# Performance work log

Measured on AMD Instinct MI355X. Metric: run time of the kernel, lower is better.

Reference implementation:

```python
import jax, jax.numpy as jnp
import numpy as np

IN_CH = 4096
OUT_CH = 11008
W_BITS = 4


def unpack_weight(qweight, wbit):
    # qweight: [in_ch * wbit // 32, out_ch] int32 -> intweight: [in_ch, out_ch] int32
    rows, cols = qweight.shape
    n = rows * (32 // wbit)
    i = jnp.arange(n)
    idx = (i * wbit) // 32            # which packed word each row comes from
    off = (i * wbit) % 32             # bit offset within the word
    # wbit=4 divides 32, so every value lies inside one word (simple path only)
    shift = (32 - off - wbit).astype(jnp.int32)
    mask = jnp.int32((1 << wbit) - 1)
    return jnp.bitwise_and(jnp.right_shift(qweight[idx], shift[:, None]), mask)


def setup_inputs() -> dict:
    key = jax.random.key(0)
    k1, k2, k3, k4 = jax.random.split(key, 4)
    x = jax.random.normal(k1, (4, 2048, IN_CH), dtype=jnp.float32)
    pack_weight = jax.random.randint(k2, (IN_CH * W_BITS // 32, OUT_CH), 0, 2**31 - 1, dtype=jnp.int32)
    w_scale = jax.random.uniform(k3, (OUT_CH, 1), dtype=jnp.float32) * 0.01 + 1e-3
    w_zero_point = jax.random.uniform(k4, (OUT_CH, 1), dtype=jnp.float32) * 15.0
    return {"x": x, "pack_weight": pack_weight, "w_scale": w_scale, "w_zero_point": w_zero_point}


def reference(x, pack_weight, w_scale, w_zero_point):
    # unpack int4 -> [in, out], transpose to [out, in] like w.t() in torch
    intw = unpack_weight(pack_weight, W_BITS).T.astype(x.dtype)  # [out, in]
    # per-channel dequant: scale/zero are [out, 1]
    w = (intw - w_zero_point) * w_scale                          # [out, in]
    # F.linear(x, w): x @ w.T
    return jnp.einsum('bsi,oi->bso', x, w)
```

## Files before the change

kernel.cpp:

```cpp
#include <hip/hip_runtime.h>
#include <hip/hip_bf16.h>


#define K_DIM 4096
#define N_DIM 11008
#define M_DIM 8192
#define LDA 40

typedef __attribute__((ext_vector_type(8))) short short8;
typedef __attribute__((ext_vector_type(4))) float f32x4;
typedef __attribute__((ext_vector_type(4))) unsigned int u32x4;

__global__ __launch_bounds__(256, 3) void qgemm_fused(
    const float* __restrict__ X, const int* __restrict__ Q,
    const float* __restrict__ SC, const float* __restrict__ ZP,
    float* __restrict__ C)
{
    __shared__ short As[128 * LDA];
    __shared__ short Bs[128 * LDA];

    const int tid  = threadIdx.x;
    const int lane = tid & 63;
    const int wave = tid >> 6;

    const int m0 = blockIdx.y * 128;
    const int n0 = blockIdx.x * 128;

    const int arow = tid >> 2;
    const int ak8  = (tid & 3) * 8;
    const float* xbase = X + (size_t)(m0 + arow) * K_DIM + ak8;

    const int bcol  = tid & 127;
    const int brow0 = tid >> 7;
    const int* qbase = Q + (size_t)brow0 * N_DIM + n0 + bcol;
    const float sc  = SC[n0 + bcol];
    const float nzs = -ZP[n0 + bcol] * sc;

    f32x4 areg[4];
    int   breg[2];

    auto load_tile = [&](int kt) {
        const float* p0 = xbase + kt;
        areg[0] = *(const f32x4*)(p0);
        areg[1] = *(const f32x4*)(p0 + 4);
        const float* p1 = p0 + (size_t)64 * K_DIM;
        areg[2] = *(const f32x4*)(p1);
        areg[3] = *(const f32x4*)(p1 + 4);
        const int* q0 = qbase + (size_t)(kt >> 3) * N_DIM;
        breg[0] = q0[0];
        breg[1] = q0[2 * N_DIM];
    };

    auto cvt2 = [&](float a, float b) -> unsigned {
        __hip_bfloat162 h = __float22bfloat162_rn(make_float2(a, b));
        unsigned u;
        __builtin_memcpy(&u, &h, 4);
        return u;
    };

    auto store_tile = [&]() {
        #pragma unroll
        for (int p = 0; p < 2; ++p) {
            u32x4 v;
            v[0] = cvt2(areg[2*p+0][0], areg[2*p+0][1]);
            v[1] = cvt2(areg[2*p+0][2], areg[2*p+0][3]);
            v[2] = cvt2(areg[2*p+1][0], areg[2*p+1][1]);
            v[3] = cvt2(areg[2*p+1][2], areg[2*p+1][3]);
            *(u32x4*)&As[(arow + p * 64) * LDA + ak8] = v;
        }
        #pragma unroll
        for (int r = 0; r < 2; ++r) {
            const unsigned w = (unsigned)breg[r];
            float f[8];
            #pragma unroll
            for (int j = 0; j < 8; ++j)
                f[j] = fmaf((float)((w >> (28 - 4*j)) & 15u), sc, nzs);
            u32x4 v;
            v[0] = cvt2(f[0], f[1]);
            v[1] = cvt2(f[2], f[3]);
            v[2] = cvt2(f[4], f[5]);
            v[3] = cvt2(f[6], f[7]);
            *(u32x4*)&Bs[bcol * LDA + (brow0 + 2*r) * 8] = v;
        }
    };

    f32x4 acc[4][4] = {};

    const int wm = (wave >> 1) * 64;
    const int wn = (wave & 1) * 64;
    const int fr = lane & 15;
    const int fq = lane >> 4;

    const short* Abase = &As[(wm + fr) * LDA + fq * 8];
    const short* Bbase = &Bs[(wn + fr) * LDA + fq * 8];

    load_tile(0);
    store_tile();
    __syncthreads();

    for (int kt = 0;;) {
        const int knext = kt + 32;
        const bool last = (knext >= K_DIM);
        if (!last) load_tile(knext);

        short8 af[4], bf[4];
        #pragma unroll
        for (int i = 0; i < 4; ++i) {
            af[i] = *(const short8*)(Abase + i * 16 * LDA);
            bf[i] = *(const short8*)(Bbase + i * 16 * LDA);
        }
        #pragma unroll
        for (int mi = 0; mi < 4; ++mi)
            #pragma unroll
            for (int ni = 0; ni < 4; ++ni)
                acc[mi][ni] = __builtin_amdgcn_mfma_f32_16x16x32_bf16(
                    af[mi], bf[ni], acc[mi][ni], 0, 0, 0);

        if (last) break;
        __syncthreads();
        store_tile();
        __syncthreads();
        kt = knext;
    }

    #pragma unroll
    for (int mi = 0; mi < 4; ++mi) {
        #pragma unroll
        for (int ni = 0; ni < 4; ++ni) {
            const int row = m0 + wm + mi * 16 + fq * 4;
            const int col = n0 + wn + ni * 16 + fr;
            float* cp = C + (size_t)row * N_DIM + col;
            #pragma unroll
            for (int r = 0; r < 4; ++r)
                cp[(size_t)r * N_DIM] = acc[mi][ni][r];
        }
    }
}

extern "C" void kernel_launch(void* const* d_in, const int* in_sizes, int n_in,
                              void* d_out, int out_size, void* d_ws, size_t ws_size,
                              hipStream_t stream) {
    const float* X  = (const float*)d_in[0];
    const int*   Q  = (const int*)d_in[1];
    const float* SC = (const float*)d_in[2];
    const float* ZP = (const float*)d_in[3];
    float*       C  = (float*)d_out;
    (void)d_ws; (void)ws_size; (void)in_sizes; (void)n_in; (void)out_size;

    qgemm_fused<<<dim3(N_DIM / 128, M_DIM / 128), 256, 0, stream>>>(X, Q, SC, ZP, C);
}
```

Measured before the change: 1.336 ms.

## Pre-convert X and dequantize weights into workspace, then run async-LDS GEMM

Splits the fused kernel into three launches. The first converts X to bf16 and the second dequantizes the int4 weights into a transposed bf16 [N,K] buffer, both written to the workspace. The third is a GEMM that streams tiles directly from global memory into double-buffered, XOR-swizzled LDS with global_load_lds. This removes the per-tile conversion and dequant work that every block repeated, and lets loads overlap compute. In exchange it costs extra global traffic and two extra launches, and it needs enough workspace, falling back to the old fused kernel otherwise.

New measurement: 1.671 ms. 25.1% more time.

```diff
diff --git a/kernel.cpp b/kernel.cpp
--- a/kernel.cpp
+++ b/kernel.cpp
@@ -5,12 +5,143 @@
 #define K_DIM 4096
 #define N_DIM 11008
 #define M_DIM 8192
-#define LDA 40
-
+#define BK 32
+
+typedef unsigned short u16;
 typedef __attribute__((ext_vector_type(8))) short short8;
 typedef __attribute__((ext_vector_type(4))) float f32x4;
 typedef __attribute__((ext_vector_type(4))) unsigned int u32x4;
 
+__device__ __forceinline__ unsigned cvt2(float a, float b) {
+    __hip_bfloat162 h = __float22bfloat162_rn(make_float2(a, b));
+    unsigned u;
+    __builtin_memcpy(&u, &h, 4);
+    return u;
+}
+
+#define GLOAD_LDS16(g, l)                                                 \
+    __builtin_amdgcn_global_load_lds(                                     \
+        (const __attribute__((address_space(1))) unsigned int*)(g),       \
+        (__attribute__((address_space(3))) unsigned int*)(l), 16, 0, 0)
+
+__global__ __launch_bounds__(256) void xcvt(const float* __restrict__ X,
+                                            u16* __restrict__ Xb) {
+    const size_t i = ((size_t)blockIdx.x * 256 + threadIdx.x) * 8;
+    f32x4 a = *(const f32x4*)(X + i);
+    f32x4 b = *(const f32x4*)(X + i + 4);
+    u32x4 v;
+    v[0] = cvt2(a[0], a[1]);
+    v[1] = cvt2(a[2], a[3]);
+    v[2] = cvt2(b[0], b[1]);
+    v[3] = cvt2(b[2], b[3]);
+    *(u32x4*)(Xb + i) = v;
+}
+
+__global__ __launch_bounds__(256) void wdeq(const int* __restrict__ Q,
+                                            const float* __restrict__ SC,
+                                            const float* __restrict__ ZP,
+                                            u16* __restrict__ Wt) {
+    const int t  = threadIdx.x;
+    const int n  = blockIdx.x * 32 + (t >> 3);
+    const int kw = blockIdx.y * 8 + (t & 7);
+    const unsigned w = (unsigned)Q[(size_t)kw * N_DIM + n];
+    const float sc  = SC[n];
+    const float nzs = -ZP[n] * sc;
+    float f[8];
+#pragma unroll
+    for (int j = 0; j < 8; ++j)
+        f[j] = fmaf((float)((w >> (28 - 4 * j)) & 15u), sc, nzs);
+    u32x4 v;
+    v[0] = cvt2(f[0], f[1]);
+    v[1] = cvt2(f[2], f[3]);
+    v[2] = cvt2(f[4], f[5]);
+    v[3] = cvt2(f[6], f[7]);
+    *(u32x4*)(Wt + (size_t)n * K_DIM + kw * 8) = v;
+}
+
+__global__ __launch_bounds__(256, 3) void qgemm_main(const u16* __restrict__ Ab,
+                                                     const u16* __restrict__ Bt,
+                                                     float* __restrict__ C) {
+    __shared__ u16 As[2][128 * BK];
+    __shared__ u16 Bs[2][128 * BK];
+
+    const int tid  = threadIdx.x;
+    const int lane = tid & 63;
+    const int wave = tid >> 6;
+    const int m0 = blockIdx.y * 128;
+    const int n0 = blockIdx.x * 128;
+
+    const int srow = tid >> 2;
+    const int sk8  = (tid & 3) ^ ((tid >> 3) & 3);
+    const u16* ga0 = Ab + (size_t)(m0 + srow) * K_DIM + sk8 * 8;
+    const u16* ga1 = ga0 + (size_t)64 * K_DIM;
+    const u16* gb0 = Bt + (size_t)(n0 + srow) * K_DIM + sk8 * 8;
+    const u16* gb1 = gb0 + (size_t)64 * K_DIM;
+
+    auto stage = [&](int buf, int kt) {
+        u16* la = &As[buf][tid * 8];
+        u16* lb = &Bs[buf][tid * 8];
+        GLOAD_LDS16(ga0 + kt, la);
+        GLOAD_LDS16(ga1 + kt, la + 2048);
+        GLOAD_LDS16(gb0 + kt, lb);
+        GLOAD_LDS16(gb1 + kt, lb + 2048);
+    };
+
+    const int wm = (wave >> 1) * 64;
+    const int wn = (wave & 1) * 64;
+    const int fr = lane & 15;
+    const int fq = lane >> 4;
+    const int sw = (fr >> 1) & 3;
+    const int aoff = (wm + fr) * BK + (fq ^ sw) * 8;
+    const int boff = (wn + fr) * BK + (fq ^ sw) * 8;
+
+    f32x4 acc[4][4] = {};
+
+    stage(0, 0);
+    __syncthreads();
+
+    int cur = 0;
+    for (int kt = 0;;) {
+        const int knext = kt + BK;
+        const bool last = (knext >= K_DIM);
+        if (!last) stage(cur ^ 1, knext);
+
+        const u16* Ap = &As[cur][aoff];
+        const u16* Bp = &Bs[cur][boff];
+        short8 af[4], bf[4];
+#pragma unroll
+        for (int i = 0; i < 4; ++i) {
+            af[i] = *(const short8*)(Ap + i * 16 * BK);
+            bf[i] = *(const short8*)(Bp + i * 16 * BK);
+        }
+#pragma unroll
+        for (int mi = 0; mi < 4; ++mi)
+#pragma unroll
+            for (int ni = 0; ni < 4; ++ni)
+                acc[mi][ni] = __builtin_amdgcn_mfma_f32_16x16x32_bf16(
+                    af[mi], bf[ni], acc[mi][ni], 0, 0, 0);
+
+        if (last) break;
+        __syncthreads();
+        cur ^= 1;
+        kt = knext;
+    }
+
+#pragma unroll
+    for (int mi = 0; mi < 4; ++mi) {
+#pragma unroll
+        for (int ni = 0; ni < 4; ++ni) {
+            const int row = m0 + wm + mi * 16 + fq * 4;
+            const int col = n0 + wn + ni * 16 + fr;
+            float* cp = C + (size_t)row * N_DIM + col;
+#pragma unroll
+            for (int r = 0; r < 4; ++r)
+                cp[(size_t)r * N_DIM] = acc[mi][ni][r];
+        }
+    }
+}
+
+#define LDA 40
 __global__ __launch_bounds__(256, 3) void qgemm_fused(
     const float* __restrict__ X, const int* __restrict__ Q,
     const float* __restrict__ SC, const float* __restrict__ ZP,
@@ -49,13 +180,6 @@
         const int* q0 = qbase + (size_t)(kt >> 3) * N_DIM;
         breg[0] = q0[0];
         breg[1] = q0[2 * N_DIM];
-    };
-
-    auto cvt2 = [&](float a, float b) -> unsigned {
-        __hip_bfloat162 h = __float22bfloat162_rn(make_float2(a, b));
-        unsigned u;
-        __builtin_memcpy(&u, &h, 4);
-        return u;
     };
 
     auto store_tile = [&]() {
@@ -145,7 +269,18 @@
     const float* SC = (const float*)d_in[2];
     const float* ZP = (const float*)d_in[3];
     float*       C  = (float*)d_out;
-    (void)d_ws; (void)ws_size; (void)in_sizes; (void)n_in; (void)out_size;
-
-    qgemm_fused<<<dim3(N_DIM / 128, M_DIM / 128), 256, 0, stream>>>(X, Q, SC, ZP, C);
-}
+    (void)in_sizes; (void)n_in; (void)out_size;
+
+    const size_t xb_bytes = (size_t)M_DIM * K_DIM * 2;
+    const size_t wt_bytes = (size_t)N_DIM * K_DIM * 2;
+
+    if (ws_size >= xb_bytes + wt_bytes) {
+        u16* Xb = (u16*)d_ws;
+        u16* Wt = (u16*)((char*)d_ws + xb_bytes);
+        xcvt<<<dim3(M_DIM * K_DIM / (256 * 8)), 256, 0, stream>>>(X, Xb);
+        wdeq<<<dim3(N_DIM / 32, K_DIM / 64), 256, 0, stream>>>(Q, SC, ZP, Wt);
+        qgemm_main<<<dim3(N_DIM / 128, M_DIM / 128), 256, 0, stream>>>(Xb, Wt, C);
+    } else {
+        qgemm_fused<<<dim3(N_DIM / 128, M_DIM / 128), 256, 0, stream>>>(X, Q, SC, ZP, C);
+    }
+}
```
